# Kernel tuning notes

Hardware: AMD Instinct MI355X
Metric: run time of the kernel (lower is better)

## Reference

```python
import jax, jax.numpy as jnp
import numpy as np

BN_EPS = 1e-5


def setup_inputs() -> dict:
    key = jax.random.key(0)
    ks = jax.random.split(key, 8)
    N, C, T, V, M = 32, 64, 300, 25, 2
    O, S = 64, 3  # out_channels, num_subset
    x = jax.random.normal(ks[0], (N, C, T, V, M), jnp.float32)
    PA = jax.random.normal(ks[1], (S, V, V), jnp.float32) * 0.1
    conv_w = jax.random.normal(ks[2], (O * S, C), jnp.float32) * (1.0 / np.sqrt(C))
    conv_b = jax.random.normal(ks[3], (O * S,), jnp.float32) * 0.01
    bn_gamma = jnp.ones((O,), jnp.float32)
    bn_beta = jnp.zeros((O,), jnp.float32)
    bn_mean = jax.random.normal(ks[4], (O,), jnp.float32) * 0.1
    bn_var = jax.random.uniform(ks[5], (O,), jnp.float32, 0.5, 1.5)
    return {"x": x, "PA": PA, "conv_w": conv_w, "conv_b": conv_b,
            "bn_gamma": bn_gamma, "bn_beta": bn_beta,
            "bn_mean": bn_mean, "bn_var": bn_var}


def reference(x, PA, conv_w, conv_b, bn_gamma, bn_beta, bn_mean, bn_var):
    N, C, T, V, M = x.shape
    S = PA.shape[0]
    O = conv_w.shape[0] // S
    # (N, C, T, V, M) -> (N*M, C, T, V)
    xb = jnp.transpose(x, (0, 4, 1, 2, 3)).reshape(N * M, C, T, V)
    res = xb  # identity residual (in_channels == out_channels, stride == 1)
    # 1x1 conv == per-position matmul over channels
    y = jnp.einsum('bctv,oc->botv', xb, conv_w) + conv_b[None, :, None, None]
    y = y.reshape(N * M, S, O, T, V)
    # sum over subsets of per-subset adjacency mixes (fused einsum)
    z = jnp.einsum('bsctv,svw->bctw', y, PA)
    # BatchNorm2d (inference form with running stats)
    scale = bn_gamma / jnp.sqrt(bn_var + BN_EPS)
    z = z * scale[None, :, None, None] + (bn_beta - bn_mean * scale)[None, :, None, None]
    z = jax.nn.relu(z)
    out = jax.nn.relu(z + res)
    # (N*M, O, T, V) -> (N, O, T, V, M)
    return jnp.transpose(out.reshape(N, M, O, T, V), (0, 2, 3, 4, 1))
```

## Files before the change

kernel.cpp:

```cpp
#include <hip/hip_runtime.h>
#include <cstddef>
#include <cstdint>

#define N_  32
#define C_  64
#define T_  300
#define V_  25
#define M_  2
#define S_  3
#define O_  64
#define OS_ 192
#define TB  6
#define NT_BLK (T_/TB)
#define CTVM (C_*T_*V_*M_)
#define TVM  (T_*V_*M_)
#define VM   (V_*M_)
#define XPITCH 72
#define YPITCH 72

typedef short  short8  __attribute__((ext_vector_type(8)));
typedef float  float4_ __attribute__((ext_vector_type(4)));
typedef unsigned short ushort4_ __attribute__((ext_vector_type(4)));

__device__ __forceinline__ short f2bf(float f) {
    uint32_t u = __float_as_uint(f);
    u += 0x7FFFu + ((u >> 16) & 1u);
    return (short)(u >> 16);
}
__device__ __forceinline__ unsigned pk2bf(float a, float b) {
    const uint32_t ua = (uint32_t)(uint16_t)f2bf(a);
    const uint32_t ub = (uint32_t)(uint16_t)f2bf(b);
    return ua | (ub << 16);
}
__device__ __forceinline__ float bf2f(unsigned short u) {
    return __uint_as_float(((unsigned)u) << 16);
}

__global__ void stgcn_prep(const float* __restrict__ Wc, const float* __restrict__ PA,
                           const float* __restrict__ g,  const float* __restrict__ b,
                           const float* __restrict__ mn, const float* __restrict__ vr,
                           short* __restrict__ Wb, short* __restrict__ PAb,
                           float* __restrict__ scl, float* __restrict__ sft)
{
    const int i = blockIdx.x * 256 + threadIdx.x;
    if (i < OS_ * C_) Wb[i] = f2bf(Wc[i]);
    const int r = i - OS_ * C_;
    if (r >= 0 && r < S_ * 32 * 32) {
        const int s = r >> 10, rem = r & 1023, wp = rem >> 5, vp = rem & 31;
        const float val = (wp < V_ && vp < V_) ? PA[s * V_ * V_ + vp * V_ + wp] : 0.0f;
        PAb[r] = f2bf(val);
    }
    const int q = r - S_ * 32 * 32;
    if (q >= 0 && q < O_) {
        const float sc = g[q] * rsqrtf(vr[q] + 1e-5f);
        scl[q] = sc;
        sft[q] = b[q] - mn[q] * sc;
    }
}

__global__ __launch_bounds__(256, 4)
void stgcn_main(const float* __restrict__ x, const float* __restrict__ cb,
                const short* __restrict__ Wb, const short* __restrict__ PAb,
                const float* __restrict__ sclg, const float* __restrict__ sftg,
                float* __restrict__ out)
{
    __shared__ short Xb[64 * XPITCH];
    __shared__ short Ys[OS_ * YPITCH];
    __shared__ float sclS[O_], sftS[O_];

    const int tid  = threadIdx.x;
    const int wv   = tid >> 6;
    const int lane = tid & 63;
    const int quad = lane >> 4;
    const int l15  = lane & 15;

    const int n  = blockIdx.x / NT_BLK;
    const int t0 = (blockIdx.x % NT_BLK) * TB;
    const size_t xbase = (size_t)n * CTVM;

    for (int i = tid; i < 14 * XPITCH; i += 256) {
        const int pr = i / XPITCH, cc = i - pr * XPITCH;
        const int pos = (pr < 7) ? (25 + pr) : (50 + pr);
        Xb[pos * XPITCH + cc] = 0;
    }
    if (tid < O_) { sclS[tid] = sclg[tid]; sftS[tid] = sftg[tid]; }

    const int wbase = wv * 48;
    short8 aW[3][2];
    #pragma unroll
    for (int mt = 0; mt < 3; ++mt)
        #pragma unroll
        for (int ks = 0; ks < 2; ++ks)
            aW[mt][ks] = *(const short8*)(Wb + (wbase + mt * 16 + l15) * C_ + ks * 32 + quad * 8);

    float cbw[3];
    #pragma unroll
    for (int mt = 0; mt < 3; ++mt) cbw[mt] = cb[wbase + mt * 16 + l15];

    const int oh = wv >> 1, hh = wv & 1;
    const int wc = hh * 16 + l15;
    short8 bP[3];
    #pragma unroll
    for (int s = 0; s < 3; ++s)
        bP[s] = *(const short8*)(PAb + s * 1024 + wc * 32 + quad * 8);

    {
        const float* xt = x + xbase + (size_t)t0 * VM;
        #pragma unroll
        for (int k = 0; k < 4; ++k) {
            const int p = tid + k * 256;
            if (p < 800) {
                const int v = p % 25, cp = p / 25;
                const float2 f0 = *(const float2*)(xt + (size_t)(2 * cp)     * TVM + v * 2);
                const float2 f1 = *(const float2*)(xt + (size_t)(2 * cp + 1) * TVM + v * 2);
                ((unsigned*)Xb)[v * 36 + cp]        = pk2bf(f0.x, f1.x);
                ((unsigned*)Xb)[(32 + v) * 36 + cp] = pk2bf(f0.y, f1.y);
            }
        }
    }

    for (int tt = 0; tt < TB; ++tt) {
        __syncthreads();

        float2 R0[4], R1[4];
        const bool pf = (tt + 1 < TB);
        if (pf) {
            const float* xt = x + xbase + (size_t)(t0 + tt + 1) * VM;
            #pragma unroll
            for (int k = 0; k < 4; ++k) {
                const int p = tid + k * 256;
                if (p < 800) {
                    const int v = p % 25, cp = p / 25;
                    R0[k] = *(const float2*)(xt + (size_t)(2 * cp)     * TVM + v * 2);
                    R1[k] = *(const float2*)(xt + (size_t)(2 * cp + 1) * TVM + v * 2);
                }
            }
        }

        short8 bX[4][2];
        #pragma unroll
        for (int nt = 0; nt < 4; ++nt)
            #pragma unroll
            for (int ks = 0; ks < 2; ++ks)
                bX[nt][ks] = *(const short8*)(Xb + (nt * 16 + l15) * XPITCH + ks * 32 + quad * 8);

        ushort4_ res[2][2];
        #pragma unroll
        for (int otl = 0; otl < 2; ++otl)
            #pragma unroll
            for (int m = 0; m < 2; ++m)
                res[otl][m] = *(const ushort4_*)(Xb + (m * 32 + wc) * XPITCH + (oh * 2 + otl) * 16 + quad * 4);

        #pragma unroll
        for (int mt = 0; mt < 3; ++mt) {
            #pragma unroll
            for (int nt = 0; nt < 4; ++nt) {
                float4_ acc = { cbw[mt], cbw[mt], cbw[mt], cbw[mt] };
                acc = __builtin_amdgcn_mfma_f32_16x16x32_bf16(bX[nt][0], aW[mt][0], acc, 0, 0, 0);
                acc = __builtin_amdgcn_mfma_f32_16x16x32_bf16(bX[nt][1], aW[mt][1], acc, 0, 0, 0);
                const int os = wbase + mt * 16 + l15;
                *(uint2*)(Ys + os * YPITCH + nt * 16 + quad * 4) =
                    make_uint2(pk2bf(acc[0], acc[1]), pk2bf(acc[2], acc[3]));
            }
        }
        __syncthreads();

        float4_ z[2][2];
        #pragma unroll
        for (int otl = 0; otl < 2; ++otl)
            #pragma unroll
            for (int m = 0; m < 2; ++m) { z[otl][m][0]=0.f; z[otl][m][1]=0.f; z[otl][m][2]=0.f; z[otl][m][3]=0.f; }
        #pragma unroll
        for (int s = 0; s < 3; ++s) {
            #pragma unroll
            for (int otl = 0; otl < 2; ++otl) {
                #pragma unroll
                for (int m = 0; m < 2; ++m) {
                    const short8 aY = *(const short8*)(Ys + (s * 64 + (oh * 2 + otl) * 16 + l15) * YPITCH + m * 32 + quad * 8);
                    z[otl][m] = __builtin_amdgcn_mfma_f32_16x16x32_bf16(aY, bP[s], z[otl][m], 0, 0, 0);
                }
            }
        }

        if (pf) {
            #pragma unroll
            for (int k = 0; k < 4; ++k) {
                const int p = tid + k * 256;
                if (p < 800) {
                    const int v = p % 25, cp = p / 25;
                    ((unsigned*)Xb)[v * 36 + cp]        = pk2bf(R0[k].x, R1[k].x);
                    ((unsigned*)Xb)[(32 + v) * 36 + cp] = pk2bf(R0[k].y, R1[k].y);
                }
            }
        }

        const int t = t0 + tt;
        if (wc < V_) {
            #pragma unroll
            for (int otl = 0; otl < 2; ++otl) {
                #pragma unroll
                for (int r = 0; r < 4; ++r) {
                    const int o = (oh * 2 + otl) * 16 + quad * 4 + r;
                    const float sc = sclS[o], sh = sftS[o];
                    float q0 = fmaf(z[otl][0][r], sc, sh);
                    q0 = fmaxf(q0, 0.0f);
                    q0 = fmaxf(q0 + bf2f((unsigned short)res[otl][0][r]), 0.0f);
                    float q1 = fmaf(z[otl][1][r], sc, sh);
                    q1 = fmaxf(q1, 0.0f);
                    q1 = fmaxf(q1 + bf2f((unsigned short)res[otl][1][r]), 0.0f);
                    *(float2*)(out + xbase + (size_t)o * TVM + (size_t)t * VM + wc * 2) =
                        make_float2(q0, q1);
                }
            }
        }
    }
}

extern "C" void kernel_launch(void* const* d_in, const int* in_sizes, int n_in,
                              void* d_out, int out_size, void* d_ws, size_t ws_size,
                              hipStream_t stream)
{
    const float* x    = (const float*)d_in[0];
    const float* PA   = (const float*)d_in[1];
    const float* Wc   = (const float*)d_in[2];
    const float* cb   = (const float*)d_in[3];
    const float* bn_g = (const float*)d_in[4];
    const float* bn_b = (const float*)d_in[5];
    const float* bn_m = (const float*)d_in[6];
    const float* bn_v = (const float*)d_in[7];
    float* out = (float*)d_out;

    char* ws = (char*)d_ws;
    short* Wb  = (short*)ws;
    short* PAb = (short*)(ws + 24576);
    float* scl = (float*)(ws + 30720);
    float* sft = (float*)(ws + 30976);

    stgcn_prep<<<61, 256, 0, stream>>>(Wc, PA, bn_g, bn_b, bn_m, bn_v, Wb, PAb, scl, sft);
    stgcn_main<<<N_ * NT_BLK, 256, 0, stream>>>(x, cb, Wb, PAb, scl, sft, out);
}
```

Before: 342.3 us.

## Load two timesteps per iteration with float4 global loads into double X tile

The shared X tile doubles so it holds two consecutive timesteps. Each prefetch now issues 16-byte float4 loads that cover two t values at once, since the 50-float V*M rows are contiguous across t. The prefetch runs only on odd iterations, and its conversion to bf16 moves to after the output stores. This gives wider, more coalesced global reads and halves the number of prefetch phases, at the cost of more LDS, higher register pressure and an occupancy hint lowered from 4 to 3.

```diff
diff --git a/kernel.cpp b/kernel.cpp
--- a/kernel.cpp
+++ b/kernel.cpp
@@ -58,13 +58,13 @@
     }
 }
 
-__global__ __launch_bounds__(256, 4)
+__global__ __launch_bounds__(256, 3)
 void stgcn_main(const float* __restrict__ x, const float* __restrict__ cb,
                 const short* __restrict__ Wb, const short* __restrict__ PAb,
                 const float* __restrict__ sclg, const float* __restrict__ sftg,
                 float* __restrict__ out)
 {
-    __shared__ short Xb[64 * XPITCH];
+    __shared__ short Xb[128 * XPITCH];
     __shared__ short Ys[OS_ * YPITCH];
     __shared__ float sclS[O_], sftS[O_];
 
@@ -78,9 +78,10 @@
     const int t0 = (blockIdx.x % NT_BLK) * TB;
     const size_t xbase = (size_t)n * CTVM;
 
-    for (int i = tid; i < 14 * XPITCH; i += 256) {
+    for (int i = tid; i < 28 * XPITCH; i += 256) {
         const int pr = i / XPITCH, cc = i - pr * XPITCH;
-        const int pos = (pr < 7) ? (25 + pr) : (50 + pr);
+        const int g  = pr / 7, w = pr - g * 7;
+        const int pos = (g >> 1) * 64 + (g & 1) * 32 + 25 + w;
         Xb[pos * XPITCH + cc] = 0;
     }
     if (tid < O_) { sclS[tid] = sclg[tid]; sftS[tid] = sftg[tid]; }
@@ -105,16 +106,22 @@
         bP[s] = *(const short8*)(PAb + s * 1024 + wc * 32 + quad * 8);
 
     {
-        const float* xt = x + xbase + (size_t)t0 * VM;
+        const float* xp = x + xbase + (size_t)t0 * VM;
         #pragma unroll
         for (int k = 0; k < 4; ++k) {
-            const int p = tid + k * 256;
+            const int p = tid + (k << 8);
             if (p < 800) {
-                const int v = p % 25, cp = p / 25;
-                const float2 f0 = *(const float2*)(xt + (size_t)(2 * cp)     * TVM + v * 2);
-                const float2 f1 = *(const float2*)(xt + (size_t)(2 * cp + 1) * TVM + v * 2);
-                ((unsigned*)Xb)[v * 36 + cp]        = pk2bf(f0.x, f1.x);
-                ((unsigned*)Xb)[(32 + v) * 36 + cp] = pk2bf(f0.y, f1.y);
+                const int cp = p / 25, q = p - cp * 25;
+                const float4_ F0 = *(const float4_*)(xp + (size_t)(2 * cp)     * TVM + q * 4);
+                const float4_ F1 = *(const float4_*)(xp + (size_t)(2 * cp + 1) * TVM + q * 4);
+                #pragma unroll
+                for (int j = 0; j < 4; ++j) {
+                    const int f  = 4 * q + j;
+                    const int dt = (f >= 50) ? 1 : 0;
+                    const int r  = f - 50 * dt;
+                    const int row = dt * 64 + (r & 1) * 32 + (r >> 1);
+                    ((unsigned*)Xb)[row * 36 + cp] = pk2bf(F0[j], F1[j]);
+                }
             }
         }
     }
@@ -122,34 +129,35 @@
     for (int tt = 0; tt < TB; ++tt) {
         __syncthreads();
 
-        float2 R0[4], R1[4];
-        const bool pf = (tt + 1 < TB);
+        float4_ P0[4], P1[4];
+        const bool pf = (tt & 1) && (tt + 1 < TB);
         if (pf) {
-            const float* xt = x + xbase + (size_t)(t0 + tt + 1) * VM;
+            const float* xp = x + xbase + (size_t)(t0 + tt + 1) * VM;
             #pragma unroll
             for (int k = 0; k < 4; ++k) {
-                const int p = tid + k * 256;
+                const int p = tid + (k << 8);
                 if (p < 800) {
-                    const int v = p % 25, cp = p / 25;
-                    R0[k] = *(const float2*)(xt + (size_t)(2 * cp)     * TVM + v * 2);
-                    R1[k] = *(const float2*)(xt + (size_t)(2 * cp + 1) * TVM + v * 2);
-                }
-            }
-        }
-
+                    const int cp = p / 25, q = p - cp * 25;
+                    P0[k] = *(const float4_*)(xp + (size_t)(2 * cp)     * TVM + q * 4);
+                    P1[k] = *(const float4_*)(xp + (size_t)(2 * cp + 1) * TVM + q * 4);
+                }
+            }
+        }
+
+        const short* Xc = Xb + (tt & 1) * (64 * XPITCH);
         short8 bX[4][2];
         #pragma unroll
         for (int nt = 0; nt < 4; ++nt)
             #pragma unroll
             for (int ks = 0; ks < 2; ++ks)
-                bX[nt][ks] = *(const short8*)(Xb + (nt * 16 + l15) * XPITCH + ks * 32 + quad * 8);
+                bX[nt][ks] = *(const short8*)(Xc + (nt * 16 + l15) * XPITCH + ks * 32 + quad * 8);
 
         ushort4_ res[2][2];
         #pragma unroll
         for (int otl = 0; otl < 2; ++otl)
             #pragma unroll
             for (int m = 0; m < 2; ++m)
-                res[otl][m] = *(const ushort4_*)(Xb + (m * 32 + wc) * XPITCH + (oh * 2 + otl) * 16 + quad * 4);
+                res[otl][m] = *(const ushort4_*)(Xc + (m * 32 + wc) * XPITCH + (oh * 2 + otl) * 16 + quad * 4);
 
         #pragma unroll
         for (int mt = 0; mt < 3; ++mt) {
@@ -178,18 +186,6 @@
                 for (int m = 0; m < 2; ++m) {
                     const short8 aY = *(const short8*)(Ys + (s * 64 + (oh * 2 + otl) * 16 + l15) * YPITCH + m * 32 + quad * 8);
                     z[otl][m] = __builtin_amdgcn_mfma_f32_16x16x32_bf16(aY, bP[s], z[otl][m], 0, 0, 0);
-                }
-            }
-        }
-
-        if (pf) {
-            #pragma unroll
-            for (int k = 0; k < 4; ++k) {
-                const int p = tid + k * 256;
-                if (p < 800) {
-                    const int v = p % 25, cp = p / 25;
-                    ((unsigned*)Xb)[v * 36 + cp]        = pk2bf(R0[k].x, R1[k].x);
-                    ((unsigned*)Xb)[(32 + v) * 36 + cp] = pk2bf(R0[k].y, R1[k].y);
                 }
             }
         }
@@ -213,6 +209,24 @@
                 }
             }
         }
+
+        if (pf) {
+            #pragma unroll
+            for (int k = 0; k < 4; ++k) {
+                const int p = tid + (k << 8);
+                if (p < 800) {
+                    const int cp = p / 25, q = p - cp * 25;
+                    #pragma unroll
+                    for (int j = 0; j < 4; ++j) {
+                        const int f  = 4 * q + j;
+                        const int dt = (f >= 50) ? 1 : 0;
+                        const int r  = f - 50 * dt;
+                        const int row = dt * 64 + (r & 1) * 32 + (r >> 1);
+                        ((unsigned*)Xb)[row * 36 + cp] = pk2bf(P0[k][j], P1[k][j]);
+                    }
+                }
+            }
+        }
     }
 }
 
```

Result: slower. 374.0 us (+9.3%).

## Stream x tiles via global_load_lds double buffer with manual waitcnt pipelining

Applied to the files above, without the earlier changes.

Replaces the register-staged x prefetch and bf16 repack with direct global-to-LDS DMA loads of raw fp32 tiles into a two-deep LDS ring. Operands are converted to bf16 when read from LDS, and the residual is now read in fp32. Loads are issued two timesteps ahead and synchronised with hand-written vmcnt waits and barriers. The aim is to overlap global loads with MFMA work and free VGPRs. In exchange, LDS use grows, which lowers the occupancy target to 3, and the hand-counted waits are fragile if the load count changes.

```diff
diff --git a/kernel.cpp b/kernel.cpp
--- a/kernel.cpp
+++ b/kernel.cpp
@@ -15,12 +15,11 @@
 #define CTVM (C_*T_*V_*M_)
 #define TVM  (T_*V_*M_)
 #define VM   (V_*M_)
-#define XPITCH 72
+#define XTILE (C_*VM)
 #define YPITCH 72
 
 typedef short  short8  __attribute__((ext_vector_type(8)));
 typedef float  float4_ __attribute__((ext_vector_type(4)));
-typedef unsigned short ushort4_ __attribute__((ext_vector_type(4)));
 
 __device__ __forceinline__ short f2bf(float f) {
     uint32_t u = __float_as_uint(f);
@@ -28,12 +27,33 @@
     return (short)(u >> 16);
 }
 __device__ __forceinline__ unsigned pk2bf(float a, float b) {
-    const uint32_t ua = (uint32_t)(uint16_t)f2bf(a);
-    const uint32_t ub = (uint32_t)(uint16_t)f2bf(b);
-    return ua | (ub << 16);
-}
-__device__ __forceinline__ float bf2f(unsigned short u) {
-    return __uint_as_float(((unsigned)u) << 16);
+    unsigned ua = __float_as_uint(a), ub = __float_as_uint(b);
+    ua += 0x7FFFu + ((ua >> 16) & 1u);
+    ub += 0x7FFFu + ((ub >> 16) & 1u);
+    return __builtin_amdgcn_perm(ub, ua, 0x07060302u);
+}
+
+#define WAITV_LG(N) asm volatile("s_waitcnt vmcnt(" #N ") lgkmcnt(0)" ::: "memory")
+#define WAIT_LG()   asm volatile("s_waitcnt lgkmcnt(0)" ::: "memory")
+#define BARRIER()   do { __builtin_amdgcn_s_barrier(); asm volatile("" ::: "memory"); } while (0)
+
+__device__ __forceinline__ void dma_tile(const float* __restrict__ xt, float* dst,
+                                         int wv, int lane)
+{
+    #pragma unroll
+    for (int i = 0; i < 13; ++i) {
+        const int q = wv + 4 * i;
+        if (q < 50) {
+            const unsigned f = (unsigned)(q * 64 + lane);
+            const unsigned c = f / 50u;
+            const unsigned r = f - c * 50u;
+            const float* g = xt + (size_t)c * TVM + r;
+            __builtin_amdgcn_global_load_lds(
+                (const __attribute__((address_space(1))) void*)g,
+                (__attribute__((address_space(3))) void*)(dst + q * 64),
+                4, 0, 0);
+        }
+    }
 }
 
 __global__ void stgcn_prep(const float* __restrict__ Wc, const float* __restrict__ PA,
@@ -58,13 +78,13 @@
     }
 }
 
-__global__ __launch_bounds__(256, 4)
+__global__ __launch_bounds__(256, 3)
 void stgcn_main(const float* __restrict__ x, const float* __restrict__ cb,
                 const short* __restrict__ Wb, const short* __restrict__ PAb,
                 const float* __restrict__ sclg, const float* __restrict__ sftg,
                 float* __restrict__ out)
 {
-    __shared__ short Xb[64 * XPITCH];
+    __shared__ float Xf[2 * XTILE];
     __shared__ short Ys[OS_ * YPITCH];
     __shared__ float sclS[O_], sftS[O_];
 
@@ -78,11 +98,6 @@
     const int t0 = (blockIdx.x % NT_BLK) * TB;
     const size_t xbase = (size_t)n * CTVM;
 
-    for (int i = tid; i < 14 * XPITCH; i += 256) {
-        const int pr = i / XPITCH, cc = i - pr * XPITCH;
-        const int pos = (pr < 7) ? (25 + pr) : (50 + pr);
-        Xb[pos * XPITCH + cc] = 0;
-    }
     if (tid < O_) { sclS[tid] = sclg[tid]; sftS[tid] = sftg[tid]; }
 
     const int wbase = wv * 48;
@@ -104,52 +119,50 @@
     for (int s = 0; s < 3; ++s)
         bP[s] = *(const short8*)(PAb + s * 1024 + wc * 32 + quad * 8);
 
-    {
-        const float* xt = x + xbase + (size_t)t0 * VM;
-        #pragma unroll
-        for (int k = 0; k < 4; ++k) {
-            const int p = tid + k * 256;
-            if (p < 800) {
-                const int v = p % 25, cp = p / 25;
-                const float2 f0 = *(const float2*)(xt + (size_t)(2 * cp)     * TVM + v * 2);
-                const float2 f1 = *(const float2*)(xt + (size_t)(2 * cp + 1) * TVM + v * 2);
-                ((unsigned*)Xb)[v * 36 + cp]        = pk2bf(f0.x, f1.x);
-                ((unsigned*)Xb)[(32 + v) * 36 + cp] = pk2bf(f0.y, f1.y);
-            }
-        }
-    }
+    dma_tile(x + xbase + (size_t)t0 * VM,       Xf,         wv, lane);
+    dma_tile(x + xbase + (size_t)(t0 + 1) * VM, Xf + XTILE, wv, lane);
 
     for (int tt = 0; tt < TB; ++tt) {
-        __syncthreads();
-
-        float2 R0[4], R1[4];
-        const bool pf = (tt + 1 < TB);
-        if (pf) {
-            const float* xt = x + xbase + (size_t)(t0 + tt + 1) * VM;
-            #pragma unroll
-            for (int k = 0; k < 4; ++k) {
-                const int p = tid + k * 256;
-                if (p < 800) {
-                    const int v = p % 25, cp = p / 25;
-                    R0[k] = *(const float2*)(xt + (size_t)(2 * cp)     * TVM + v * 2);
-                    R1[k] = *(const float2*)(xt + (size_t)(2 * cp + 1) * TVM + v * 2);
-                }
-            }
-        }
+        if (wv < 2) {
+            if      (tt == 0) WAITV_LG(13);
+            else if (tt == 1) WAITV_LG(21);
+            else if (tt <  5) WAITV_LG(29);
+            else              WAITV_LG(16);
+        } else {
+            if      (tt == 0) WAITV_LG(12);
+            else if (tt == 1) WAITV_LG(20);
+            else if (tt <  5) WAITV_LG(28);
+            else              WAITV_LG(16);
+        }
+        BARRIER();
+
+        const float* Xc = Xf + (tt & 1) * XTILE;
 
         short8 bX[4][2];
         #pragma unroll
-        for (int nt = 0; nt < 4; ++nt)
-            #pragma unroll
-            for (int ks = 0; ks < 2; ++ks)
-                bX[nt][ks] = *(const short8*)(Xb + (nt * 16 + l15) * XPITCH + ks * 32 + quad * 8);
-
-        ushort4_ res[2][2];
+        for (int nt = 0; nt < 4; ++nt) {
+            const int pos = nt * 16 + l15;
+            const int vm  = (pos & 31) * 2 + (pos >> 5);
+            const unsigned keep = ((pos & 31) < V_) ? 0xFFFFFFFFu : 0u;
+            #pragma unroll
+            for (int ks = 0; ks < 2; ++ks) {
+                const float* pb = Xc + (ks * 32 + quad * 8) * VM + vm;
+                union { short8 s; unsigned u[4]; } U;
+                #pragma unroll
+                for (int j2 = 0; j2 < 4; ++j2)
+                    U.u[j2] = pk2bf(pb[(2 * j2) * VM], pb[(2 * j2 + 1) * VM]) & keep;
+                bX[nt][ks] = U.s;
+            }
+        }
+
+        float2 resv[2][4];
         #pragma unroll
         for (int otl = 0; otl < 2; ++otl)
             #pragma unroll
-            for (int m = 0; m < 2; ++m)
-                res[otl][m] = *(const ushort4_*)(Xb + (m * 32 + wc) * XPITCH + (oh * 2 + otl) * 16 + quad * 4);
+            for (int r = 0; r < 4; ++r) {
+                const int o = (oh * 2 + otl) * 16 + quad * 4 + r;
+                resv[otl][r] = *(const float2*)(Xc + o * VM + wc * 2);
+            }
 
         #pragma unroll
         for (int mt = 0; mt < 3; ++mt) {
@@ -163,7 +176,12 @@
                     make_uint2(pk2bf(acc[0], acc[1]), pk2bf(acc[2], acc[3]));
             }
         }
-        __syncthreads();
+
+        WAIT_LG();
+        BARRIER();
+
+        if (tt + 2 < TB)
+            dma_tile(x + xbase + (size_t)(t0 + tt + 2) * VM, Xf + (tt & 1) * XTILE, wv, lane);
 
         float4_ z[2][2];
         #pragma unroll
@@ -178,18 +196,6 @@
                 for (int m = 0; m < 2; ++m) {
                     const short8 aY = *(const short8*)(Ys + (s * 64 + (oh * 2 + otl) * 16 + l15) * YPITCH + m * 32 + quad * 8);
                     z[otl][m] = __builtin_amdgcn_mfma_f32_16x16x32_bf16(aY, bP[s], z[otl][m], 0, 0, 0);
-                }
-            }
-        }
-
-        if (pf) {
-            #pragma unroll
-            for (int k = 0; k < 4; ++k) {
-                const int p = tid + k * 256;
-                if (p < 800) {
-                    const int v = p % 25, cp = p / 25;
-                    ((unsigned*)Xb)[v * 36 + cp]        = pk2bf(R0[k].x, R1[k].x);
-                    ((unsigned*)Xb)[(32 + v) * 36 + cp] = pk2bf(R0[k].y, R1[k].y);
                 }
             }
         }
@@ -204,10 +210,10 @@
                     const float sc = sclS[o], sh = sftS[o];
                     float q0 = fmaf(z[otl][0][r], sc, sh);
                     q0 = fmaxf(q0, 0.0f);
-                    q0 = fmaxf(q0 + bf2f((unsigned short)res[otl][0][r]), 0.0f);
+                    q0 = fmaxf(q0 + resv[otl][r].x, 0.0f);
                     float q1 = fmaf(z[otl][1][r], sc, sh);
                     q1 = fmaxf(q1, 0.0f);
-                    q1 = fmaxf(q1 + bf2f((unsigned short)res[otl][1][r]), 0.0f);
+                    q1 = fmaxf(q1 + resv[otl][r].y, 0.0f);
                     *(float2*)(out + xbase + (size_t)o * TVM + (size_t)t * VM + wc * 2) =
                         make_float2(q0, q1);
                 }
```

Measured after the change: 403.7 us. 17.9% more time.
